# Kernel optimization log

Hardware: AMD Instinct MI355X
Metric: run time of the kernel (lower is better)

Reference implementation:

```python
import math
import jax, jax.numpy as jnp
import numpy as np

D_MODEL = 256
N_HEADS = 8
D_K = D_MODEL // N_HEADS
BS = 2
SEQ = 2048
NEG = -1e32


def _linear(x, W, b):
    return x @ W + b


def _layernorm(x, g, b):
    m = jnp.mean(x, axis=-1, keepdims=True)
    v = jnp.mean((x - m) ** 2, axis=-1, keepdims=True)
    return (x - m) / jnp.sqrt(v + 1e-5) * g + b


def _attention(q, k, v, mask, gammas):
    # q,k,v: [b,h,s,dk]; mask: [1,1,s,s] bool; gammas: [h,1,1]
    d_k = q.shape[-1]
    scores = jnp.einsum('bhqd,bhkd->bhqk', q, k) / math.sqrt(d_k)
    S = scores.shape[-1]
    # distance-decay bias (computed under stop_gradient, as torch.no_grad + detach)
    sm = jax.lax.stop_gradient(jax.nn.softmax(jnp.where(mask, scores, NEG), axis=-1))
    distcum = jnp.cumsum(sm, axis=-1)
    disttot = jnp.sum(sm, axis=-1, keepdims=True)
    idx = jnp.arange(S, dtype=scores.dtype)
    pos = jnp.abs(idx[None, :] - idx[:, None])[None, None]  # |i-j|
    dist = jax.lax.stop_gradient(
        jnp.sqrt(jnp.clip((disttot - distcum) * pos, 0.0, None)))
    gamma = -jax.nn.softplus(gammas)[None]  # [1,h,1,1]
    eff = jnp.clip(jnp.exp(dist * gamma), 1e-5, 1e5)
    scores = jnp.where(mask, scores * eff, NEG)
    scores = jnp.where(mask, jax.nn.softmax(scores, axis=-1), 0.0)
    return jnp.einsum('bhqk,bhkd->bhqd', scores, v)


def _mha(qx, kx, vx, Wq, bq, Wk, bk, Wv, bv, Wo, bo, gammas, mask):
    bs = qx.shape[0]
    def split(x, W, b):
        return _linear(x, W, b).reshape(bs, -1, N_HEADS, D_K).transpose(0, 2, 1, 3)
    q = split(qx, Wq, bq)
    k = split(kx, Wk, bk)
    v = split(vx, Wv, bv)
    o = _attention(q, k, v, mask, gammas)
    o = o.transpose(0, 2, 1, 3).reshape(bs, -1, D_MODEL)
    return _linear(o, Wo, bo)


def _layer(query, key, values, Wq, bq, Wk, bk, Wv, bv, Wo, bo, gammas, ln_g, ln_b, peek_cur):
    S = query.shape[1]
    mask = jnp.tril(jnp.ones((S, S), dtype=bool), 0 if peek_cur else -1)[None, None]
    out = _mha(query, key, values, Wq, bq, Wk, bk, Wv, bv, Wo, bo, gammas, mask)
    return _layernorm(query + out, ln_g, ln_b)


def _forward(q_emb, qa_emb,
             b1_Wq, b1_bq, b1_Wv, b1_bv, b1_Wo, b1_bo, b1_gam, b1_lng, b1_lnb,
             b2_Wq, b2_bq, b2_Wv, b2_bv, b2_Wo, b2_bo, b2_gam, b2_lng, b2_lnb,
             b3_Wq, b3_bq, b3_Wk, b3_bk, b3_Wv, b3_bv, b3_Wo, b3_bo, b3_gam, b3_lng, b3_lnb,
             know_params, lk_W, lk_b, lv_W, lv_b):
    # blocks 1 & 2: kq_same -> k projection shares q projection weights
    hq = _layer(q_emb, q_emb, q_emb,
                b1_Wq, b1_bq, b1_Wq, b1_bq, b1_Wv, b1_bv, b1_Wo, b1_bo,
                b1_gam, b1_lng, b1_lnb, peek_cur=True)
    ha = _layer(qa_emb, qa_emb, qa_emb,
                b2_Wq, b2_bq, b2_Wq, b2_bq, b2_Wv, b2_bv, b2_Wo, b2_bo,
                b2_gam, b2_lng, b2_lnb, peek_cur=True)
    query = jnp.broadcast_to(know_params, hq.shape)
    h = _layer(query, hq, ha,
               b3_Wq, b3_bq, b3_Wk, b3_bk, b3_Wv, b3_bv, b3_Wo, b3_bo,
               b3_gam, b3_lng, b3_lnb, peek_cur=False)
    bs, S, d = hq.shape
    key = jax.nn.sigmoid(_linear(
        jnp.broadcast_to(know_params, (bs, S, d)).reshape(bs, S, N_HEADS, D_K),
        lk_W, lk_b)).reshape(bs * S, N_HEADS, d)
    value = jax.nn.sigmoid(_linear(
        h.reshape(bs, S, N_HEADS, D_K), lv_W, lv_b)).reshape(bs * S, N_HEADS, d)
    beta = jnp.einsum('nhd,nd->nh', key, q_emb.reshape(bs * S, d))
    alpha = jax.nn.softmax(beta, axis=-1)
    h = jnp.einsum('nh,nhd->nd', alpha, value).reshape(bs, S, d)
    return h


def setup_inputs() -> dict:
    keys = iter(jax.random.split(jax.random.key(0), 64))
    def nrm(shape, scale=0.02):
        return jax.random.normal(next(keys), shape, dtype=jnp.float32) * scale
    def uni(shape):
        return jax.random.uniform(next(keys), shape, dtype=jnp.float32, minval=-1.0, maxval=1.0)
    d = D_MODEL
    inp = {
        'q_emb': nrm((BS, SEQ, d), 1.0),
        'qa_emb': nrm((BS, SEQ, d), 1.0),
    }
    for blk in ('b1', 'b2'):
        inp[blk + '_Wq'] = nrm((d, d)); inp[blk + '_bq'] = jnp.zeros((d,), jnp.float32)
        inp[blk + '_Wv'] = nrm((d, d)); inp[blk + '_bv'] = jnp.zeros((d,), jnp.float32)
        inp[blk + '_Wo'] = nrm((d, d)); inp[blk + '_bo'] = jnp.zeros((d,), jnp.float32)
        inp[blk + '_gam'] = uni((N_HEADS, 1, 1))
        inp[blk + '_lng'] = jnp.ones((d,), jnp.float32)
        inp[blk + '_lnb'] = jnp.zeros((d,), jnp.float32)
    inp['b3_Wq'] = nrm((d, d)); inp['b3_bq'] = jnp.zeros((d,), jnp.float32)
    inp['b3_Wk'] = nrm((d, d)); inp['b3_bk'] = jnp.zeros((d,), jnp.float32)
    inp['b3_Wv'] = nrm((d, d)); inp['b3_bv'] = jnp.zeros((d,), jnp.float32)
    inp['b3_Wo'] = nrm((d, d)); inp['b3_bo'] = jnp.zeros((d,), jnp.float32)
    inp['b3_gam'] = uni((N_HEADS, 1, 1))
    inp['b3_lng'] = jnp.ones((d,), jnp.float32)
    inp['b3_lnb'] = jnp.zeros((d,), jnp.float32)
    inp['know_params'] = uni((1, 1, d))
    inp['lk_W'] = nrm((D_K, d)); inp['lk_b'] = jnp.zeros((d,), jnp.float32)
    inp['lv_W'] = nrm((D_K, d)); inp['lv_b'] = jnp.zeros((d,), jnp.float32)
    return inp


def reference(q_emb, qa_emb,
              b1_Wq, b1_bq, b1_Wv, b1_bv, b1_Wo, b1_bo, b1_gam, b1_lng, b1_lnb,
              b2_Wq, b2_bq, b2_Wv, b2_bv, b2_Wo, b2_bo, b2_gam, b2_lng, b2_lnb,
              b3_Wq, b3_bq, b3_Wk, b3_bk, b3_Wv, b3_bv, b3_Wo, b3_bo, b3_gam, b3_lng, b3_lnb,
              know_params, lk_W, lk_b, lv_W, lv_b):
    return _forward(q_emb, qa_emb,
                    b1_Wq, b1_bq, b1_Wv, b1_bv, b1_Wo, b1_bo, b1_gam, b1_lng, b1_lnb,
                    b2_Wq, b2_bq, b2_Wv, b2_bv, b2_Wo, b2_bo, b2_gam, b2_lng, b2_lnb,
                    b3_Wq, b3_bq, b3_Wk, b3_bk, b3_Wv, b3_bv, b3_Wo, b3_bo, b3_gam, b3_lng, b3_lnb,
                    know_params, lk_W, lk_b, lv_W, lv_b)
```

## Files before the change

kernel.cpp:

```cpp
#include <hip/hip_runtime.h>
#include <hip/hip_bf16.h>

#define DM 256
#define NH 8
#define DK 32
#define BSZ 2
#define SEQ 2048
#define ROWS (BSZ*SEQ)
#define RT 16
#define SRB 2312

static __device__ __forceinline__ int sw8(int j) { return j + ((j >> 6) << 3); }

typedef __attribute__((ext_vector_type(8))) short short8;
typedef __attribute__((ext_vector_type(4))) float f32x4;

static __device__ __forceinline__ unsigned short f2bf(float f) {
    unsigned u = __float_as_uint(f);
    return (unsigned short)((u + 0x7FFFu + ((u >> 16) & 1u)) >> 16);
}
static __device__ __forceinline__ float bf2f(unsigned short h) {
    return __uint_as_float(((unsigned)h) << 16);
}

static __device__ __forceinline__ unsigned cvtpk(float lo, float hi) {
    unsigned r;
    asm("v_cvt_pk_bf16_f32 %0, %1, %2" : "=v"(r) : "v"(lo), "v"(hi));
    return r;
}

static __device__ __forceinline__ float ex2(float x) { return __builtin_amdgcn_exp2f(x); }
static __device__ __forceinline__ float sqt(float x) { return __builtin_amdgcn_sqrtf(x); }
static __device__ __forceinline__ float rcp(float x) { return __builtin_amdgcn_rcpf(x); }

template<int CTRL, int RM>
static __device__ __forceinline__ float dppadd(float x) {
    int s = __builtin_amdgcn_update_dpp(0, __float_as_int(x), CTRL, RM, 0xf, true);
    return x + __int_as_float(s);
}
static __device__ __forceinline__ float scan32(float x) {
    x = dppadd<0x111, 0xf>(x);
    x = dppadd<0x112, 0xf>(x);
    x = dppadd<0x114, 0xf>(x);
    x = dppadd<0x118, 0xf>(x);
    x = dppadd<0x142, 0xa>(x);
    return x;
}
static __device__ __forceinline__ float red16(float x) {
    x = dppadd<0x0B1, 0xf>(x);
    x = dppadd<0x04E, 0xf>(x);
    x = dppadd<0x124, 0xf>(x);
    x = dppadd<0x128, 0xf>(x);
    return x;
}
static __device__ __forceinline__ float bcast31(float x) {
    return __int_as_float(__builtin_amdgcn_ds_swizzle(__float_as_int(x), 0x03E0));
}
static __device__ __forceinline__ float swz_x16(float x) {
    return __int_as_float(__builtin_amdgcn_ds_swizzle(__float_as_int(x), 0x401F));
}

static __device__ __forceinline__ void unpack4(uint2 u, float& s0, float& s1,
                                               float& s2, float& s3) {
    s0 = __uint_as_float(u.x << 16);
    s1 = __uint_as_float(u.x & 0xFFFF0000u);
    s2 = __uint_as_float(u.y << 16);
    s3 = __uint_as_float(u.y & 0xFFFF0000u);
}

static __device__ __forceinline__ uint2 decay_quad(
    float s0, float s1, float s2, float s3v,
    float e0, float e1, float e2, float e3,
    float cum, float pq, float linv,
    float l, float gamma2, float& l2)
{
    float p0, p1, p2, p3;
    cum += e0;
    { float dist = sqt(fmaxf((l - cum) * pq, 0.f));
      float eff = fmaxf(ex2(dist * gamma2), 1e-5f);
      p0 = ex2(s0 * eff); l2 += p0; }
    cum += e1;
    { float dist = sqt(fmaxf((l - cum) * (pq - linv), 0.f));
      float eff = fmaxf(ex2(dist * gamma2), 1e-5f);
      p1 = ex2(s1 * eff); l2 += p1; }
    cum += e2;
    { float dist = sqt(fmaxf((l - cum) * (pq - 2.f * linv), 0.f));
      float eff = fmaxf(ex2(dist * gamma2), 1e-5f);
      p2 = ex2(s2 * eff); l2 += p2; }
    cum += e3;
    { float dist = sqt(fmaxf((l - cum) * (pq - 3.f * linv), 0.f));
      float eff = fmaxf(ex2(dist * gamma2), 1e-5f);
      p3 = ex2(s3v * eff); l2 += p3; }
    uint2 st;
    st.x = cvtpk(p0, p1);
    st.y = cvtpk(p2, p3);
    return st;
}

#define MFMA_BF16 __builtin_amdgcn_mfma_f32_16x16x32_bf16
#define LOG2E 1.44269504088896340736f

static __device__ __forceinline__ float waveRedSum(float v) {
    #pragma unroll
    for (int off = 32; off > 0; off >>= 1) v += __shfl_down(v, off, 64);
    return v;
}

__global__ __launch_bounds__(256) void convert_w_kernel(
    const float* __restrict__ S0, const float* __restrict__ S1, const float* __restrict__ S2,
    const float* __restrict__ S3, const float* __restrict__ S4, const float* __restrict__ S5,
    const float* __restrict__ S6, const float* __restrict__ S7, const float* __restrict__ S8,
    unsigned short* __restrict__ dst,
    const float* __restrict__ know,
    const float* __restrict__ W3q, const float* __restrict__ b3q,
    const float* __restrict__ lkW, const float* __restrict__ lkb,
    float* __restrict__ q3row, float* __restrict__ key8)
{
    __shared__ float kn[DM];
    int s = blockIdx.y;
    if (s == 9) {
        if (blockIdx.x != 0) return;
        int t = threadIdx.x;
        kn[t] = know[t];
        __syncthreads();
        float acc = b3q[t];
        for (int c = 0; c < DM; ++c) acc += kn[c] * W3q[(size_t)c * DM + t];
        q3row[t] = acc;
        float bk = lkb[t];
        for (int h = 0; h < NH; ++h) {
            float a = bk;
            #pragma unroll
            for (int c = 0; c < DK; ++c) a += kn[h * DK + c] * lkW[(size_t)c * DM + t];
            key8[(size_t)h * DM + t] = 1.f / (1.f + __expf(-a));
        }
        return;
    }
    const float* W;
    if (s == 0) W = S0; else if (s == 1) W = S1; else if (s == 2) W = S2;
    else if (s == 3) W = S3; else if (s == 4) W = S4; else if (s == 5) W = S5;
    else if (s == 6) W = S6; else if (s == 7) W = S7; else W = S8;
    unsigned short* H = dst + (size_t)s * 131072;
    unsigned short* L = H + 65536;

    int e = blockIdx.x * 1024 + threadIdx.x * 4;
    int k = e >> 8, n = e & 255;
    float4 w4 = *(const float4*)(W + e);
    float v[4] = {w4.x, w4.y, w4.z, w4.w};
    #pragma unroll
    for (int i = 0; i < 4; ++i) {
        unsigned short h = f2bf(v[i]);
        H[(size_t)(n + i) * 256 + k] = h;
        L[(size_t)(n + i) * 256 + k] = (unsigned short)f2bf(v[i] - bf2f(h));
    }
}

__global__ __launch_bounds__(256) void gemm4_kernel(
    const float* __restrict__ X0, const unsigned short* __restrict__ H0, const float* __restrict__ B0,
    float* __restrict__ Y0, unsigned short* __restrict__ K0o, unsigned short* __restrict__ V0o,
    const float* __restrict__ X1, const unsigned short* __restrict__ H1, const float* __restrict__ B1,
    float* __restrict__ Y1, unsigned short* __restrict__ K1o, unsigned short* __restrict__ V1o,
    const float* __restrict__ X2, const unsigned short* __restrict__ H2, const float* __restrict__ B2,
    float* __restrict__ Y2, unsigned short* __restrict__ K2o, unsigned short* __restrict__ V2o,
    const float* __restrict__ X3, const unsigned short* __restrict__ H3, const float* __restrict__ B3,
    float* __restrict__ Y3, unsigned short* __restrict__ K3o, unsigned short* __restrict__ V3o)
{
    const float *X, *Bias; const unsigned short* H; float* Yf;
    unsigned short *KSo, *VSo;
    int s = blockIdx.y;
    if (s == 0)      { X = X0; H = H0; Bias = B0; Yf = Y0; KSo = K0o; VSo = V0o; }
    else if (s == 1) { X = X1; H = H1; Bias = B1; Yf = Y1; KSo = K1o; VSo = V1o; }
    else if (s == 2) { X = X2; H = H2; Bias = B2; Yf = Y2; KSo = K2o; VSo = V2o; }
    else             { X = X3; H = H3; Bias = B3; Yf = Y3; KSo = K3o; VSo = V3o; }
    const unsigned short* L = H + 65536;

    __shared__ __align__(16) unsigned short XhL[16 * 264];
    __shared__ __align__(16) unsigned short XlL[16 * 264];
    int t = threadIdx.x;
    int r0 = blockIdx.x * 16;
    {
        int r = t >> 4, c0 = (t & 15) * 16;
        const float* xp = X + (size_t)(r0 + r) * DM + c0;
        #pragma unroll
        for (int i = 0; i < 16; i += 4) {
            float4 v4 = *(const float4*)(xp + i);
            float vv[4] = {v4.x, v4.y, v4.z, v4.w};
            #pragma unroll
            for (int j = 0; j < 4; ++j) {
                unsigned short h = f2bf(vv[j]);
                XhL[r * 264 + c0 + i + j] = h;
                XlL[r * 264 + c0 + i + j] = (unsigned short)f2bf(vv[j] - bf2f(h));
            }
        }
    }
    __syncthreads();
    int lane = t & 63, wv = t >> 6;
    int m = lane & 15, quad = lane >> 4;
    f32x4 aa[4];
    #pragma unroll
    for (int nt = 0; nt < 4; ++nt) { aa[nt][0]=0.f; aa[nt][1]=0.f; aa[nt][2]=0.f; aa[nt][3]=0.f; }
    #pragma unroll 1
    for (int kc = 0; kc < 8; ++kc) {
        int k0 = kc * 32;
        short8 Ah = *(const short8*)&XhL[m * 264 + k0 + quad * 8];
        short8 Al = *(const short8*)&XlL[m * 264 + k0 + quad * 8];
        size_t boff = (size_t)(wv * 64 + m) * 256 + k0 + quad * 8;
        #pragma unroll
        for (int nt = 0; nt < 4; ++nt) {
            short8 Bh = *(const short8*)(H + boff + nt * 16 * 256);
            short8 Bl = *(const short8*)(L + boff + nt * 16 * 256);
            aa[nt] = MFMA_BF16(Al, Bh, aa[nt], 0, 0, 0);
            aa[nt] = MFMA_BF16(Ah, Bl, aa[nt], 0, 0, 0);
            aa[nt] = MFMA_BF16(Ah, Bh, aa[nt], 0, 0, 0);
        }
    }
    int col0 = wv * 64 + m;
    #pragma unroll
    for (int nt = 0; nt < 4; ++nt) {
        int col = col0 + nt * 16;
        float bb = Bias[col];
        float yv[4];
        #pragma unroll
        for (int g = 0; g < 4; ++g) yv[g] = aa[nt][g] + bb;
        if (Yf) {
            #pragma unroll
            for (int g = 0; g < 4; ++g)
                Yf[(size_t)(r0 + quad * 4 + g) * DM + col] = yv[g];
        }
        if (KSo) {
            unsigned short* KH = KSo;
            unsigned short* KL = KSo + (size_t)ROWS * DM;
            #pragma unroll
            for (int g = 0; g < 4; ++g) {
                unsigned short hb = f2bf(yv[g]);
                KH[(size_t)(r0 + quad * 4 + g) * DM + col] = hb;
                KL[(size_t)(r0 + quad * 4 + g) * DM + col] =
                    (unsigned short)f2bf(yv[g] - bf2f(hb));
            }
        }
        if (VSo) {
            unsigned short* VH = VSo;
            ushort4 h4;
            h4.x = f2bf(yv[0]); h4.y = f2bf(yv[1]);
            h4.z = f2bf(yv[2]); h4.w = f2bf(yv[3]);
            *(ushort4*)&VH[(size_t)col * ROWS + r0 + quad * 4] = h4;
        }
    }
}

__global__ __launch_bounds__(256) void gemm_ln2_kernel(
    const float* __restrict__ X0, const unsigned short* __restrict__ H0, const float* __restrict__ B0,
    const float* __restrict__ R0, const float* __restrict__ G0, const float* __restrict__ L0,
    float* __restrict__ Y0, int bc0,
    const float* __restrict__ X1, const unsigned short* __restrict__ H1, const float* __restrict__ B1,
    const float* __restrict__ R1, const float* __restrict__ G1, const float* __restrict__ L1,
    float* __restrict__ Y1, int bc1)
{
    const float *X, *Bias, *R, *G, *Lb; const unsigned short* H; float* Y; int bc;
    if (blockIdx.y == 0) { X=X0; H=H0; Bias=B0; R=R0; G=G0; Lb=L0; Y=Y0; bc=bc0; }
    else                 { X=X1; H=H1; Bias=B1; R=R1; G=G1; Lb=L1; Y=Y1; bc=bc1; }
    const unsigned short* L = H + 65536;

    __shared__ __align__(16) unsigned short XhL[16 * 264];
    __shared__ __align__(16) unsigned short XlL[16 * 264];
    __shared__ __align__(16) float yl[16 * 260];
    int t = threadIdx.x;
    int r0 = blockIdx.x * 16;
    {   int r = t >> 4, c0 = (t & 15) * 16;
        const float* xp = X + (size_t)(r0 + r) * DM + c0;
        #pragma unroll
        for (int i = 0; i < 16; i += 4) {
            float4 v4 = *(const float4*)(xp + i);
            float vv[4] = {v4.x, v4.y, v4.z, v4.w};
            #pragma unroll
            for (int j = 0; j < 4; ++j) {
                unsigned short h = f2bf(vv[j]);
                XhL[r * 264 + c0 + i + j] = h;
                XlL[r * 264 + c0 + i + j] = (unsigned short)f2bf(vv[j] - bf2f(h));
            }
        }
    }
    __syncthreads();
    int lane = t & 63, wv = t >> 6;
    int m = lane & 15, quad = lane >> 4;
    f32x4 aa[4];
    #pragma unroll
    for (int nt = 0; nt < 4; ++nt) { aa[nt][0]=0.f; aa[nt][1]=0.f; aa[nt][2]=0.f; aa[nt][3]=0.f; }
    #pragma unroll 1
    for (int kc = 0; kc < 8; ++kc) {
        int k0 = kc * 32;
        short8 Ah = *(const short8*)&XhL[m * 264 + k0 + quad * 8];
        short8 Al = *(const short8*)&XlL[m * 264 + k0 + quad * 8];
        size_t boff = (size_t)(wv * 64 + m) * 256 + k0 + quad * 8;
        #pragma unroll
        for (int nt = 0; nt < 4; ++nt) {
            short8 Bh = *(const short8*)(H + boff + nt * 16 * 256);
            short8 Bl = *(const short8*)(L + boff + nt * 16 * 256);
            aa[nt] = MFMA_BF16(Al, Bh, aa[nt], 0, 0, 0);
            aa[nt] = MFMA_BF16(Ah, Bl, aa[nt], 0, 0, 0);
            aa[nt] = MFMA_BF16(Ah, Bh, aa[nt], 0, 0, 0);
        }
    }
    {
        int col0 = wv * 64 + m;
        #pragma unroll
        for (int nt = 0; nt < 4; ++nt) {
            int col = col0 + nt * 16;
            float bb = Bias[col];
            #pragma unroll
            for (int g = 0; g < 4; ++g) {
                int row = quad * 4 + g;
                float res = bc ? R[col] : R[(size_t)(r0 + row) * DM + col];
                yl[row * 260 + col] = aa[nt][g] + bb + res;
            }
        }
    }
    __syncthreads();
    {
        int r = t >> 4, c0 = (t & 15) * 16;
        float vals[16];
        float part = 0.f;
        #pragma unroll
        for (int i = 0; i < 16; ++i) { vals[i] = yl[r * 260 + c0 + i]; part += vals[i]; }
        #pragma unroll
        for (int off = 8; off; off >>= 1) part += __shfl_xor(part, off, 16);
        float mean = part * (1.f / DM);
        float vp = 0.f;
        #pragma unroll
        for (int i = 0; i < 16; ++i) { float d = vals[i] - mean; vp += d * d; }
        #pragma unroll
        for (int off = 8; off; off >>= 1) vp += __shfl_xor(vp, off, 16);
        float rs = rsqrtf(vp * (1.f / DM) + 1e-5f);
        float* yp = Y + (size_t)(r0 + r) * DM + c0;
        #pragma unroll
        for (int i = 0; i < 16; i += 4) {
            float4 o;
            o.x = (vals[i+0] - mean) * rs * G[c0+i+0] + Lb[c0+i+0];
            o.y = (vals[i+1] - mean) * rs * G[c0+i+1] + Lb[c0+i+1];
            o.z = (vals[i+2] - mean) * rs * G[c0+i+2] + Lb[c0+i+2];
            o.w = (vals[i+3] - mean) * rs * G[c0+i+3] + Lb[c0+i+3];
            *(float4*)(yp + i) = o;
        }
    }
}

__global__ __launch_bounds__(256) void score3a_kernel(
    const float* __restrict__ q3row, const float* __restrict__ K3,
    unsigned short* __restrict__ S3, float* __restrict__ C3,
    float* __restrict__ Csum)
{
    __shared__ float wsum[4];
    int s = blockIdx.x;
    int bh = blockIdx.y;
    int b = bh >> 3, h = bh & 7;
    int t = threadIdx.x;
    int lane = t & 63, wv = t >> 6;
    int j = s * 256 + t;
    const float scaleL2 = 0.17677669529663687f * LOG2E;
    float qv[DK];
    #pragma unroll
    for (int d = 0; d < DK; d += 4) {
        float4 qq = *(const float4*)(q3row + h * DK + d);
        qv[d+0] = qq.x * scaleL2; qv[d+1] = qq.y * scaleL2;
        qv[d+2] = qq.z * scaleL2; qv[d+3] = qq.w * scaleL2;
    }
    const float* kp = K3 + ((size_t)b * SEQ + j) * DM + h * DK;
    float kv[DK];
    #pragma unroll
    for (int d = 0; d < DK; d += 4) {
        float4 kq = *(const float4*)(kp + d);
        kv[d+0] = kq.x; kv[d+1] = kq.y; kv[d+2] = kq.z; kv[d+3] = kq.w;
    }
    float sc = 0.f;
    #pragma unroll
    for (int d = 0; d < DK; ++d) sc += qv[d] * kv[d];
    unsigned short sb16 = f2bf(sc);
    float e = ex2(bf2f(sb16));
    float x = e;
    #pragma unroll
    for (int off = 1; off < 64; off <<= 1) {
        float y = __shfl_up(x, off, 64);
        if (lane >= off) x += y;
    }
    if (lane == 63) wsum[wv] = x;
    __syncthreads();
    float woff = 0.f;
    for (int w = 0; w < wv; ++w) woff += wsum[w];
    float inc = woff + x;
    S3[(size_t)bh * SEQ + j] = sb16;
    C3[(size_t)bh * SEQ + j] = inc;
    if (t == 255) Csum[bh * 8 + s] = inc;
}

__global__ __launch_bounds__(256) void score3b_kernel(
    const float* __restrict__ Csum, float* __restrict__ C3)
{
    int s = blockIdx.x + 1;
    int bh = blockIdx.y;
    int t = threadIdx.x;
    float off = 0.f;
    for (int w = 0; w < s; ++w) off += Csum[bh * 8 + w];
    C3[(size_t)bh * SEQ + s * 256 + t] += off;
}

__global__ __launch_bounds__(512) void attn_tile_kernel(
    const float* __restrict__ Q0,
    const unsigned short* __restrict__ KS0, const unsigned short* __restrict__ VS0,
    const float* __restrict__ g0, float* __restrict__ O0,
    const float* __restrict__ Q1,
    const unsigned short* __restrict__ KS1, const unsigned short* __restrict__ VS1,
    const float* __restrict__ g1, float* __restrict__ O1,
    const unsigned short* __restrict__ S3g, const float* __restrict__ C3g,
    int peek, int qbcast)
{
    __shared__ __align__(16) unsigned short SB[RT * SRB];
    __shared__ float qs[RT][DK];
    __shared__ float l2inv_s[RT];
    __shared__ float rowsum[8 * RT];

    int bx, by;
    {
        int flat = (int)blockIdx.y * 128 + (int)blockIdx.x;
        int per = ((int)gridDim.y * 128) >> 3;
        int nf = (flat & 7) * per + (flat >> 3);
        by = nf >> 7;
        bx = nf & 127;
    }
    int y = by;
    int set = y >> 4, bh = y & 15;
    const float* Q = set ? Q1 : Q0;
    const unsigned short* KS = set ? KS1 : KS0;
    const unsigned short* VS = set ? VS1 : VS0;
    const float* gm = set ? g1 : g0;
    float* O = set ? O1 : O0;

    int b = bh >> 3, h = bh & 7;
    int i0 = (127 - bx) * RT;
    int t = threadIdx.x;
    size_t base = ((size_t)b * SEQ) * DM + (size_t)h * DK;

    int njAll = peek ? (i0 + RT) : (i0 + RT - 1);
    int njPad32 = (njAll + 31) & ~31;
    int njPad128 = (njAll + 127) & ~127;
    const float scaleL2 = 0.17677669529663687f * LOG2E;

    if (!qbcast) {
        {
            int r = t >> 5, d = t & 31;
            qs[r][d] = Q[base + (size_t)(i0 + r) * DM + d];
        }
        __syncthreads();

        {
            int wave = t >> 6, lane = t & 63;
            int m = lane & 15, quad = lane >> 4;

            float av[8];
            {
                float4 qa = *(const float4*)&qs[m][8 * quad];
                float4 qb = *(const float4*)&qs[m][8 * quad + 4];
                av[0]=qa.x*scaleL2; av[1]=qa.y*scaleL2; av[2]=qa.z*scaleL2; av[3]=qa.w*scaleL2;
                av[4]=qb.x*scaleL2; av[5]=qb.y*scaleL2; av[6]=qb.z*scaleL2; av[7]=qb.w*scaleL2;
            }
            short8 Ah;
            #pragma unroll
            for (int i = 0; i < 8; ++i) Ah[i] = (short)f2bf(av[i]);

            const unsigned short* KH = KS;
            const unsigned short* KL = KS + (size_t)ROWS * DM;
            size_t rowb = (size_t)b * SEQ;
            int njr0 = i0 + quad * 4 + peek;
            float rp0 = 0.f, rp1 = 0.f, rp2 = 0.f, rp3 = 0.f;
            int nChunks = (njAll + 15) >> 4;
            #pragma unroll 2
            for (int c = wave; c < nChunks; c += 8) {
                int j0 = c << 4;
                size_t off = (rowb + j0 + m) * DM + h * DK + quad * 8;
                short8 Bh = *(const short8*)&KH[off];
                short8 Bl = *(const short8*)&KL[off];
                f32x4 acc = {0.f, 0.f, 0.f, 0.f};
                acc = MFMA_BF16(Ah, Bl, acc, 0, 0, 0);
                acc = MFMA_BF16(Ah, Bh, acc, 0, 0, 0);
                int jcol = j0 + m;
                int sj = sw8(jcol);
                unsigned pk01 = cvtpk(acc[0], acc[1]);
                unsigned pk23 = cvtpk(acc[2], acc[3]);
                SB[(quad * 4 + 0) * SRB + sj] = (unsigned short)pk01;
                SB[(quad * 4 + 1) * SRB + sj] = (unsigned short)(pk01 >> 16);
                SB[(quad * 4 + 2) * SRB + sj] = (unsigned short)pk23;
                SB[(quad * 4 + 3) * SRB + sj] = (unsigned short)(pk23 >> 16);
                rp0 += (jcol < njr0 + 0) ? ex2(acc[0]) : 0.f;
                rp1 += (jcol < njr0 + 1) ? ex2(acc[1]) : 0.f;
                rp2 += (jcol < njr0 + 2) ? ex2(acc[2]) : 0.f;
                rp3 += (jcol < njr0 + 3) ? ex2(acc[3]) : 0.f;
            }
            rp0 = red16(rp0); rp1 = red16(rp1);
            rp2 = red16(rp2); rp3 = red16(rp3);
            if (m == 0) {
                rowsum[wave * RT + quad * 4 + 0] = rp0;
                rowsum[wave * RT + quad * 4 + 1] = rp1;
                rowsum[wave * RT + quad * 4 + 2] = rp2;
                rowsum[wave * RT + quad * 4 + 3] = rp3;
            }
        }
        __syncthreads();

        {
            int r = t >> 5, c = t & 31;
            int i = i0 + r;
            int nj = peek ? (i + 1) : i;
            for (int j = nj + c; j < njPad128; j += 32)
                SB[r * SRB + sw8(j)] = 0xFF80u;
        }
        __syncthreads();
    }

    if (qbcast) {
        int r = t >> 5, c = t & 31;
        int i = i0 + r;
        int nj = peek ? (i + 1) : i;
        unsigned short* Sr = SB + r * SRB;
        float gamma2 = -log1pf(__expf(gm[h])) * LOG2E;
        const unsigned short* s3p = S3g + (size_t)bh * SEQ;
        const float* c3p = C3g + (size_t)bh * SEQ;
        float Lc = (nj > 0) ? c3p[nj - 1] : 0.f;
        float linv = (nj > 0) ? rcp(Lc) : 0.f;
        float li2 = linv + linv, li3 = li2 + linv;
        float l2 = 0.f;
        #pragma unroll 2
        for (int k = 0; 128 * k < njPad32; ++k) {
            int j4 = 128 * k + 4 * c;
            uint2 su = *(const uint2*)&s3p[j4];
            float4 C4 = *(const float4*)&c3p[j4];
            float s0 = __uint_as_float(su.x << 16);
            float s1 = __uint_as_float(su.x & 0xFFFF0000u);
            float s2 = __uint_as_float(su.y << 16);
            float s3v = __uint_as_float(su.y & 0xFFFF0000u);
            float pq = (float)(i - j4) * linv;
            float p0, p1, p2, p3;
            { float dist = sqt(fmaxf((Lc - C4.x) * pq, 0.f));
              float eff = fmaxf(ex2(dist * gamma2), 1e-5f);
              p0 = (j4 + 0 < nj) ? ex2(s0 * eff) : 0.f; l2 += p0; }
            { float dist = sqt(fmaxf((Lc - C4.y) * (pq - linv), 0.f));
              float eff = fmaxf(ex2(dist * gamma2), 1e-5f);
              p1 = (j4 + 1 < nj) ? ex2(s1 * eff) : 0.f; l2 += p1; }
            { float dist = sqt(fmaxf((Lc - C4.z) * (pq - li2), 0.f));
              float eff = fmaxf(ex2(dist * gamma2), 1e-5f);
              p2 = (j4 + 2 < nj) ? ex2(s2 * eff) : 0.f; l2 += p2; }
            { float dist = sqt(fmaxf((Lc - C4.w) * (pq - li3), 0.f));
              float eff = fmaxf(ex2(dist * gamma2), 1e-5f);
              p3 = (j4 + 3 < nj) ? ex2(s3v * eff) : 0.f; l2 += p3; }
            uint2 st;
            st.x = cvtpk(p0, p1);
            st.y = cvtpk(p2, p3);
            *(uint2*)&Sr[sw8(j4)] = st;
        }
        l2 = red16(l2);
        l2 += swz_x16(l2);
        if (c == 0) l2inv_s[r] = (nj > 0) ? rcp(l2) : 0.f;
    } else {
        int r = t >> 5, c = t & 31;
        int i = i0 + r;
        int nj = peek ? (i + 1) : i;
        unsigned short* Sr = SB + r * SRB;
        float gamma2 = -log1pf(__expf(gm[h])) * LOG2E;

        float l = 0.f;
        #pragma unroll
        for (int w = 0; w < 8; ++w) l += rowsum[w * RT + r];
        float linv = rcp(l);

        float l2 = 0.f;
        float Bc = 0.f;
        int nIter = (njPad32 + 127) >> 7;
        int pairs = nIter >> 1;
        #pragma unroll 1
        for (int k = 0; k < pairs; ++k) {
            int j4a = 256 * k + 4 * c;
            int j4b = j4a + 128;
            uint2 uA = *(const uint2*)&Sr[sw8(j4a)];
            uint2 uB = *(const uint2*)&Sr[sw8(j4b)];
            float a0, a1, a2, a3, b0, b1, b2, b3;
            unpack4(uA, a0, a1, a2, a3);
            unpack4(uB, b0, b1, b2, b3);
            float eA0 = ex2(a0), eA1 = ex2(a1), eA2 = ex2(a2), eA3 = ex2(a3);
            float eB0 = ex2(b0), eB1 = ex2(b1), eB2 = ex2(b2), eB3 = ex2(b3);
            float sigA = eA0 + eA1 + eA2 + eA3;
            float sigB = eB0 + eB1 + eB2 + eB3;
            float xA = scan32(sigA);
            float xB = scan32(sigB);
            float totA = bcast31(xA);
            float totB = bcast31(xB);
            float cumA = Bc + (xA - sigA);
            float cumB = Bc + totA + (xB - sigB);
            Bc += totA + totB;
            float pqA = (float)(i - j4a) * linv;
            float pqB = pqA - 128.f * linv;
            uint2 stA = decay_quad(a0, a1, a2, a3, eA0, eA1, eA2, eA3,
                                   cumA, pqA, linv, l, gamma2, l2);
            uint2 stB = decay_quad(b0, b1, b2, b3, eB0, eB1, eB2, eB3,
                                   cumB, pqB, linv, l, gamma2, l2);
            *(uint2*)&Sr[sw8(j4a)] = stA;
            *(uint2*)&Sr[sw8(j4b)] = stB;
        }
        if (nIter & 1) {
            int j4a = 256 * pairs + 4 * c;
            uint2 uA = *(const uint2*)&Sr[sw8(j4a)];
            float a0, a1, a2, a3;
            unpack4(uA, a0, a1, a2, a3);
            float eA0 = ex2(a0), eA1 = ex2(a1), eA2 = ex2(a2), eA3 = ex2(a3);
            float sigA = eA0 + eA1 + eA2 + eA3;
            float xA = scan32(sigA);
            float cumA = Bc + (xA - sigA);
            float pqA = (float)(i - j4a) * linv;
            uint2 stA = decay_quad(a0, a1, a2, a3, eA0, eA1, eA2, eA3,
                                   cumA, pqA, linv, l, gamma2, l2);
            *(uint2*)&Sr[sw8(j4a)] = stA;
        }
        l2 = red16(l2);
        l2 += swz_x16(l2);
        if (c == 0) l2inv_s[r] = (nj > 0) ? rcp(l2) : 0.f;
    }
    __syncthreads();

    {
        int wave = t >> 6, lane = t & 63;
        int n16 = lane & 15, quad = lane >> 4;
        const unsigned short* VH = VS;
        size_t vb0 = (size_t)(h * DK + n16) * ROWS + (size_t)b * SEQ;
        size_t vb1 = (size_t)(h * DK + 16 + n16) * ROWS + (size_t)b * SEQ;
        f32x4 oc0 = {0.f,0.f,0.f,0.f}, oc1 = {0.f,0.f,0.f,0.f};
        #pragma unroll 2
        for (int j0 = wave * 32; j0 < njPad32; j0 += 256) {
            short8 Ap = *(const short8*)&SB[n16 * SRB + sw8(j0 + quad * 8)];
            int jo = j0 + quad * 8;
            short8 Bh0 = *(const short8*)&VH[vb0 + jo];
            short8 Bh1 = *(const short8*)&VH[vb1 + jo];
            oc0 = MFMA_BF16(Ap, Bh0, oc0, 0, 0, 0);
            oc1 = MFMA_BF16(Ap, Bh1, oc1, 0, 0, 0);
        }
        __syncthreads();
        float* FS = (float*)SB;
        {
            #pragma unroll
            for (int g = 0; g < 4; ++g) {
                int row = quad * 4 + g;
                FS[wave * 512 + row * 32 + n16] = oc0[g];
                FS[wave * 512 + row * 32 + 16 + n16] = oc1[g];
            }
        }
    }
    __syncthreads();
    {
        float* FS = (float*)SB;
        int r2 = t >> 5, d = t & 31;
        float sum = 0.f;
        #pragma unroll
        for (int w = 0; w < 8; ++w)
            sum += FS[w * 512 + r2 * 32 + d];
        int ii = i0 + r2;
        O[base + (size_t)ii * DM + d] = sum * l2inv_s[r2];
    }
}

__global__ __launch_bounds__(256) void readout_kernel(
    const float* __restrict__ h3, const float* __restrict__ qe,
    const float* __restrict__ key8,
    const float* __restrict__ lvW, const float* __restrict__ lvb,
    float* __restrict__ out)
{
    __shared__ float hrow[DM], qrow[DM];
    __shared__ float red8[4][NH];
    int n = blockIdx.x, t = threadIdx.x;
    int lane = t & 63, wid = t >> 6;
    hrow[t] = h3[(size_t)n * DM + t];
    qrow[t] = qe[(size_t)n * DM + t];
    __syncthreads();
    float ph[NH];
    #pragma unroll
    for (int h = 0; h < NH; ++h) {
        float v = key8[(size_t)h * DM + t] * qrow[t];
        v = waveRedSum(v);
        ph[h] = v;
    }
    if (lane == 0) {
        #pragma unroll
        for (int h = 0; h < NH; ++h) red8[wid][h] = ph[h];
    }
    __syncthreads();
    float beta[NH];
    #pragma unroll
    for (int h = 0; h < NH; ++h)
        beta[h] = red8[0][h] + red8[1][h] + red8[2][h] + red8[3][h];
    float bv = lvb[t];
    float vh[NH];
    for (int h = 0; h < NH; ++h) {
        float a = bv;
        #pragma unroll
        for (int c = 0; c < DK; ++c) a += hrow[h * DK + c] * lvW[(size_t)c * DM + t];
        vh[h] = 1.f / (1.f + __expf(-a));
    }
    float mb = beta[0];
    #pragma unroll
    for (int h = 1; h < NH; ++h) mb = fmaxf(mb, beta[h]);
    float se = 0.f, eh[NH];
    #pragma unroll
    for (int h = 0; h < NH; ++h) { eh[h] = __expf(beta[h] - mb); se += eh[h]; }
    float sinv = 1.f / se;
    float o = 0.f;
    #pragma unroll
    for (int h = 0; h < NH; ++h) o += eh[h] * sinv * vh[h];
    out[(size_t)n * DM + t] = o;
}

extern "C" void kernel_launch(void* const* d_in, const int* in_sizes, int n_in,
                              void* d_out, int out_size, void* d_ws, size_t ws_size,
                              hipStream_t stream) {
    (void)in_sizes; (void)n_in; (void)out_size; (void)ws_size;
    const float* q_emb  = (const float*)d_in[0];
    const float* qa_emb = (const float*)d_in[1];
    const float* b1_Wq = (const float*)d_in[2];
    const float* b1_bq = (const float*)d_in[3];
    const float* b1_Wv = (const float*)d_in[4];
    const float* b1_bv = (const float*)d_in[5];
    const float* b1_Wo = (const float*)d_in[6];
    const float* b1_bo = (const float*)d_in[7];
    const float* b1_gam = (const float*)d_in[8];
    const float* b1_lng = (const float*)d_in[9];
    const float* b1_lnb = (const float*)d_in[10];
    const float* b2_Wq = (const float*)d_in[11];
    const float* b2_bq = (const float*)d_in[12];
    const float* b2_Wv = (const float*)d_in[13];
    const float* b2_bv = (const float*)d_in[14];
    const float* b2_Wo = (const float*)d_in[15];
    const float* b2_bo = (const float*)d_in[16];
    const float* b2_gam = (const float*)d_in[17];
    const float* b2_lng = (const float*)d_in[18];
    const float* b2_lnb = (const float*)d_in[19];
    const float* b3_Wq = (const float*)d_in[20];
    const float* b3_bq = (const float*)d_in[21];
    const float* b3_Wk = (const float*)d_in[22];
    const float* b3_bk = (const float*)d_in[23];
    const float* b3_Wv = (const float*)d_in[24];
    const float* b3_bv = (const float*)d_in[25];
    const float* b3_Wo = (const float*)d_in[26];
    const float* b3_bo = (const float*)d_in[27];
    const float* b3_gam = (const float*)d_in[28];
    const float* b3_lng = (const float*)d_in[29];
    const float* b3_lnb = (const float*)d_in[30];
    const float* know  = (const float*)d_in[31];
    const float* lk_W  = (const float*)d_in[32];
    const float* lk_b  = (const float*)d_in[33];
    const float* lv_W  = (const float*)d_in[34];
    const float* lv_b  = (const float*)d_in[35];

    const size_t SLAB = (size_t)ROWS * DM;
    const size_t USLAB = 2 * SLAB;
    float* A1 = (float*)d_ws;
    float* A2 = A1 + SLAB;
    float* C1 = A2 + SLAB;
    float* C2 = C1 + SLAB;
    unsigned short* KS1 = (unsigned short*)(C2 + SLAB);
    unsigned short* KS2 = KS1 + USLAB;
    unsigned short* VS1 = KS2 + USLAB;
    unsigned short* VS2 = VS1 + USLAB;
    float* q3row = (float*)(VS2 + USLAB);
    float* key8  = q3row + DM;
    unsigned short* Wsp = (unsigned short*)(key8 + NH * DM);
    unsigned short* S3buf = Wsp + (size_t)9 * 131072;
    float* C3buf = (float*)(S3buf + 16 * SEQ);
    float* Csum  = C3buf + 16 * SEQ;
    float* hq = (float*)KS1;
    float* ha = (float*)KS2;
    float* k3 = A1;
    unsigned short* VS3 = VS1;
    float* O3 = C1;
    float* h3 = C2;

    auto WH = [&](int i) { return Wsp + (size_t)i * 131072; };

    dim3 blk(256);
    dim3 ablk(512);
    dim3 agrid2(SEQ / RT, 32);
    dim3 agrid1(SEQ / RT, 16);
    dim3 rgrid(ROWS);

    convert_w_kernel<<<dim3(64, 10), blk, 0, stream>>>(
        b1_Wq, b1_Wv, b1_Wo, b2_Wq, b2_Wv, b2_Wo, b3_Wk, b3_Wv, b3_Wo, Wsp,
        know, b3_Wq, b3_bq, lk_W, lk_b, q3row, key8);

    gemm4_kernel<<<dim3(ROWS/16, 4), blk, 0, stream>>>(
        q_emb,  WH(0), b1_bq, A1,      KS1,     nullptr,
        q_emb,  WH(1), b1_bv, nullptr, nullptr, VS1,
        qa_emb, WH(3), b2_bq, A2,      KS2,     nullptr,
        qa_emb, WH(4), b2_bv, nullptr, nullptr, VS2);

    attn_tile_kernel<<<agrid2, ablk, 0, stream>>>(
        A1, KS1, VS1, b1_gam, C1,
        A2, KS2, VS2, b2_gam, C2,
        nullptr, nullptr, 1, 0);

    gemm_ln2_kernel<<<dim3(ROWS/16, 2), blk, 0, stream>>>(
        C1, WH(2), b1_bo, q_emb,  b1_lng, b1_lnb, hq, 0,
        C2, WH(5), b2_bo, qa_emb, b2_lng, b2_lnb, ha, 0);

    gemm4_kernel<<<dim3(ROWS/16, 2), blk, 0, stream>>>(
        hq, WH(6), b3_bk, k3,      nullptr, nullptr,
        ha, WH(7), b3_bv, nullptr, nullptr, VS3,
        hq, WH(6), b3_bk, k3,      nullptr, nullptr,
        hq, WH(6), b3_bk, k3,      nullptr, nullptr);

    score3a_kernel<<<dim3(8, 16), blk, 0, stream>>>(q3row, k3, S3buf, C3buf, Csum);
    score3b_kernel<<<dim3(7, 16), blk, 0, stream>>>(Csum, C3buf);

    attn_tile_kernel<<<agrid1, ablk, 0, stream>>>(
        q3row, nullptr, VS3, b3_gam, O3,
        q3row, nullptr, VS3, b3_gam, O3,
        S3buf, C3buf, 0, 1);

    gemm_ln2_kernel<<<dim3(ROWS/16, 1), blk, 0, stream>>>(
        O3, WH(8), b3_bo, know, b3_lng, b3_lnb, h3, 1,
        O3, WH(8), b3_bo, know, b3_lng, b3_lnb, h3, 1);

    readout_kernel<<<rgrid, blk, 0, stream>>>(h3, q_emb, key8, lv_W, lv_b,
                                              (float*)d_out);
}
```

Before: 420.8 us.

## Stage V-transpose stores through LDS and prefetch decay loop loads

```diff
diff --git a/kernel.cpp b/kernel.cpp
--- a/kernel.cpp
+++ b/kernel.cpp
@@ -175,6 +175,7 @@
 
     __shared__ __align__(16) unsigned short XhL[16 * 264];
     __shared__ __align__(16) unsigned short XlL[16 * 264];
+    __shared__ __align__(16) unsigned short vt[256][24];
     int t = threadIdx.x;
     int r0 = blockIdx.x * 16;
     {
@@ -238,12 +239,19 @@
             }
         }
         if (VSo) {
-            unsigned short* VH = VSo;
             ushort4 h4;
             h4.x = f2bf(yv[0]); h4.y = f2bf(yv[1]);
             h4.z = f2bf(yv[2]); h4.w = f2bf(yv[3]);
-            *(ushort4*)&VH[(size_t)col * ROWS + r0 + quad * 4] = h4;
-        }
+            *(ushort4*)&vt[col][quad * 4] = h4;
+        }
+    }
+    if (VSo) {
+        __syncthreads();
+        short8 v0 = *(const short8*)&vt[t][0];
+        short8 v1 = *(const short8*)&vt[t][8];
+        unsigned short* vp = VSo + (size_t)t * ROWS + r0;
+        *(short8*)vp = v0;
+        *(short8*)(vp + 8) = v1;
     }
 }
 
@@ -526,11 +534,20 @@
         float linv = (nj > 0) ? rcp(Lc) : 0.f;
         float li2 = linv + linv, li3 = li2 + linv;
         float l2 = 0.f;
-        #pragma unroll 2
-        for (int k = 0; 128 * k < njPad32; ++k) {
-            int j4 = 128 * k + 4 * c;
-            uint2 su = *(const uint2*)&s3p[j4];
-            float4 C4 = *(const float4*)&c3p[j4];
+        int nIt = (njPad32 + 127) >> 7;
+        int j4 = 4 * c;
+        uint2 su_a = *(const uint2*)&s3p[j4];
+        float4 C4_a = *(const float4*)&c3p[j4];
+        int jp = (j4 + 128 < SEQ - 3) ? j4 + 128 : SEQ - 4;
+        uint2 su_b = *(const uint2*)&s3p[jp];
+        float4 C4_b = *(const float4*)&c3p[jp];
+        #pragma unroll 1
+        for (int k = 0; k < nIt; ++k, j4 += 128) {
+            uint2 su = su_a; float4 C4 = C4_a;
+            su_a = su_b; C4_a = C4_b;
+            int jn = (j4 + 256 < SEQ - 3) ? j4 + 256 : SEQ - 4;
+            su_b = *(const uint2*)&s3p[jn];
+            C4_b = *(const float4*)&c3p[jn];
             float s0 = __uint_as_float(su.x << 16);
             float s1 = __uint_as_float(su.x & 0xFFFF0000u);
             float s2 = __uint_as_float(su.y << 16);
@@ -573,12 +590,17 @@
         float Bc = 0.f;
         int nIter = (njPad32 + 127) >> 7;
         int pairs = nIter >> 1;
+        uint2 nxA, nxB;
+        nxA = *(const uint2*)&Sr[sw8(4 * c)];
+        nxB = *(const uint2*)&Sr[sw8(4 * c + 128)];
         #pragma unroll 1
         for (int k = 0; k < pairs; ++k) {
             int j4a = 256 * k + 4 * c;
             int j4b = j4a + 128;
-            uint2 uA = *(const uint2*)&Sr[sw8(j4a)];
-            uint2 uB = *(const uint2*)&Sr[sw8(j4b)];
+            uint2 uA = nxA;
+            uint2 uB = nxB;
+            nxA = *(const uint2*)&Sr[sw8(j4a + 256)];
+            nxB = *(const uint2*)&Sr[sw8(j4b + 256)];
             float a0, a1, a2, a3, b0, b1, b2, b3;
             unpack4(uA, a0, a1, a2, a3);
             unpack4(uB, b0, b1, b2, b3);
@@ -604,7 +626,7 @@
         }
         if (nIter & 1) {
             int j4a = 256 * pairs + 4 * c;
-            uint2 uA = *(const uint2*)&Sr[sw8(j4a)];
+            uint2 uA = nxA;
             float a0, a1, a2, a3;
             unpack4(uA, a0, a1, a2, a3);
             float eA0 = ex2(a0), eA1 = ex2(a1), eA2 = ex2(a2), eA3 = ex2(a3);
```

Measured after the change: 420.1 us (median of 2 runs). No clear change (-0.2%).
